# Optimization experiments

Measured on AMD Instinct MI355X. Metric: run time of the kernel, lower is better.

Reference implementation:

```python
import jax, jax.numpy as jnp
import numpy as np

H = 16      # num_heads
D = 64      # nhid (per-head dim)
SL, BS = 1024, 64
DM = 1024   # keys_dim == query_dim == values_dim

def setup_inputs() -> dict:
    key = jax.random.key(0)
    k1, k2, k3, k4, k5 = jax.random.split(key, 5)
    return {
        "query":  jax.random.normal(k1, (BS, DM), dtype=jnp.float32),
        "keys":   jax.random.normal(k2, (SL, BS, DM), dtype=jnp.float32),
        "values": jax.random.normal(k3, (SL, BS, DM), dtype=jnp.float32),
        "Wq":     jax.random.normal(k4, (H * D, DM), dtype=jnp.float32) * 0.02,
        "Wk":     jax.random.normal(k5, (H * D, DM), dtype=jnp.float32) * 0.02,
    }

def reference(query, keys, values, Wq, Wk):
    bs = query.shape[0]
    sl = keys.shape[0]
    scale = jnp.asarray(np.sqrt(D), dtype=query.dtype)
    # projections (note: original module applies keys_linear to values -- a bug we replicate)
    qp = (query @ Wq.T).reshape(bs, H, D)                 # [bs, H, D]
    kp = (keys @ Wk.T).reshape(sl, bs, H, D)              # [sl, bs, H, D]
    vp = (values @ Wk.T).reshape(sl, bs, H, D)            # [sl, bs, H, D]
    # per-head scaled dot-product scores, softmax over the sequence axis (dim 0)
    scores = jnp.einsum('bhd,sbhd->sbh', qp, kp) / scale  # [sl, bs, H]
    attn = jax.nn.softmax(scores, axis=0)
    out = jnp.einsum('sbh,sbhd->bhd', attn, vp)           # [bs, H, D]
    return out.reshape(bs, H * D)
```

## Files before the change

kernel.cpp:

```cpp
#include <hip/hip_runtime.h>
#include <cstddef>
#include <cstdint>

#define NH 16
#define HD 64
#define SLEN 1024
#define NB 64
#define DMODEL 1024

#define DOT4_ACC(acc, k, q) \
  acc = fmaf((k).x, (q).x, fmaf((k).y, (q).y, fmaf((k).z, (q).z, fmaf((k).w, (q).w, (acc)))))

#define FMA4_BCAST(accv, qv, w0_, w1_, w2_, w3_) do { \
  (accv).x = fmaf((qv).x, (w0_).x, fmaf((qv).y, (w1_).x, fmaf((qv).z, (w2_).x, fmaf((qv).w, (w3_).x, (accv).x)))); \
  (accv).y = fmaf((qv).x, (w0_).y, fmaf((qv).y, (w1_).y, fmaf((qv).z, (w2_).y, fmaf((qv).w, (w3_).y, (accv).y)))); \
  (accv).z = fmaf((qv).x, (w0_).z, fmaf((qv).y, (w1_).z, fmaf((qv).z, (w2_).z, fmaf((qv).w, (w3_).z, (accv).z)))); \
  (accv).w = fmaf((qv).x, (w0_).w, fmaf((qv).y, (w1_).w, fmaf((qv).z, (w2_).w, fmaf((qv).w, (w3_).w, (accv).w)))); \
} while (0)

__device__ __forceinline__ float wred_sum(float v) {
#pragma unroll
  for (int off = 32; off; off >>= 1) v += __shfl_xor(v, off, 64);
  return v;
}

__device__ __forceinline__ void gload16(const float* g, float* lds_base) {
  __builtin_amdgcn_global_load_lds(
      (const __attribute__((address_space(1))) void*)g,
      (__attribute__((address_space(3))) void*)lds_base, 16, 0, 0);
}

__global__ __launch_bounds__(256) void k0_qp(const float* __restrict__ query,
                                             const float* __restrict__ Wq,
                                             float* __restrict__ qp) {
  const int tid = threadIdx.x;
  const int w = tid >> 6, l = tid & 63;
  const int j = blockIdx.x * 4 + w;
  const float4* wr = reinterpret_cast<const float4*>(Wq + (size_t)j * DMODEL) + l * 4;
  const float4 w0 = wr[0], w1 = wr[1], w2 = wr[2], w3 = wr[3];
  for (int b = 0; b < NB; ++b) {
    const float4* qr = reinterpret_cast<const float4*>(query + (size_t)b * DMODEL) + l * 4;
    float4 q0 = qr[0], q1 = qr[1], q2 = qr[2], q3 = qr[3];
    float s = 0.f;
    DOT4_ACC(s, w0, q0); DOT4_ACC(s, w1, q1); DOT4_ACC(s, w2, q2); DOT4_ACC(s, w3, q3);
    s = wred_sum(s);
    if (l == 0) qp[(size_t)b * DMODEL + j] = s;
  }
}

__global__ __launch_bounds__(256) void k1_qt(const float* __restrict__ qp,
                                             const float* __restrict__ Wk,
                                             float* __restrict__ qt) {
  __shared__ __align__(16) float qpl[8][HD];
  const int h = blockIdx.x & 15;
  const int b0 = (blockIdx.x >> 4) * 8;
  const int tid = threadIdx.x;
  for (int f = tid; f < 8 * HD; f += 256) {
    int bi = f >> 6, d = f & 63;
    qpl[bi][d] = qp[(size_t)(b0 + bi) * DMODEL + h * HD + d];
  }
  __syncthreads();
  const int m4 = tid * 4;
  float4 acc[8];
#pragma unroll
  for (int i = 0; i < 8; ++i) acc[i] = make_float4(0.f, 0.f, 0.f, 0.f);
  const float* wbase = Wk + (size_t)(h * HD) * DMODEL + m4;
  for (int d = 0; d < HD; d += 4) {
    float4 wk0 = *reinterpret_cast<const float4*>(wbase + (size_t)(d + 0) * DMODEL);
    float4 wk1 = *reinterpret_cast<const float4*>(wbase + (size_t)(d + 1) * DMODEL);
    float4 wk2 = *reinterpret_cast<const float4*>(wbase + (size_t)(d + 2) * DMODEL);
    float4 wk3 = *reinterpret_cast<const float4*>(wbase + (size_t)(d + 3) * DMODEL);
#pragma unroll
    for (int bi = 0; bi < 8; ++bi) {
      float4 q = *reinterpret_cast<const float4*>(&qpl[bi][d]);
      FMA4_BCAST(acc[bi], q, wk0, wk1, wk2, wk3);
    }
  }
#pragma unroll
  for (int bi = 0; bi < 8; ++bi)
    *reinterpret_cast<float4*>(qt + ((size_t)(b0 + bi) * NH + h) * DMODEL + m4) = acc[bi];
}

__global__ __launch_bounds__(128) void k2_scores(const float* __restrict__ keys,
                                                 const float* __restrict__ qt,
                                                 float* __restrict__ scp) {
  __shared__ __align__(16) float ql[NH][512];
  __shared__ __align__(16) float kb[128 * 16];
  const int b  = blockIdx.x & 63;
  const int st = (blockIdx.x >> 6) & 7;
  const int mh = blockIdx.x >> 9;
  const int tid = threadIdx.x, w = tid >> 6, l = tid & 63;
  const int hg = l & 3;
  const int sg = l >> 2;
  for (int f = tid; f < NH * 128; f += 128) {
    int hh = f >> 7, m4 = (f & 127) * 4;
    *reinterpret_cast<float4*>(&ql[hh][m4]) = *reinterpret_cast<const float4*>(
        qt + ((size_t)b * NH + hh) * DMODEL + mh * 512 + m4);
  }
  const int s0 = st * 128;
  const size_t rowstride = (size_t)NB * DMODEL;
  const float* kbase = keys + ((size_t)s0 * NB + b) * DMODEL + mh * 512;
  const int srow  = l >> 2;
  const int sslot = (l & 3) ^ (srow & 3);
  float acc[4][NH];
#pragma unroll
  for (int si = 0; si < 4; ++si)
#pragma unroll
    for (int hh = 0; hh < NH; ++hh) acc[si][hh] = 0.f;
  const int sl0 = w * 64 + sg;

  for (int ch = 0; ch < 32; ++ch) {
#pragma unroll
    for (int i = 0; i < 4; ++i) {
      const int u = w * 4 + i;
      const int row = u * 16 + srow;
      const float* g = kbase + (size_t)row * rowstride + ch * 16 + sslot * 4;
      gload16(g, &kb[u * 256]);
    }
    __syncthreads();
    float4 kv[4];
#pragma unroll
    for (int si = 0; si < 4; ++si) {
      const int s = sl0 + si * 16;
      kv[si] = *reinterpret_cast<const float4*>(&kb[s * 16 + ((hg ^ (s & 3)) << 2)]);
    }
#pragma unroll
    for (int hh = 0; hh < NH; ++hh) {
      float4 q = *reinterpret_cast<const float4*>(&ql[hh][ch * 16 + hg * 4]);
      DOT4_ACC(acc[0][hh], kv[0], q);
      DOT4_ACC(acc[1][hh], kv[1], q);
      DOT4_ACC(acc[2][hh], kv[2], q);
      DOT4_ACC(acc[3][hh], kv[3], q);
    }
    __syncthreads();
  }
#pragma unroll
  for (int si = 0; si < 4; ++si)
#pragma unroll
    for (int hh = 0; hh < NH; ++hh) {
      acc[si][hh] += __shfl_xor(acc[si][hh], 1, 64);
      acc[si][hh] += __shfl_xor(acc[si][hh], 2, 64);
    }
  const float scale = 0.125f;
  float* plane = scp + (size_t)mh * NB * NH * SLEN;
#pragma unroll
  for (int j = 0; j < 4; ++j) {
#pragma unroll
    for (int si = 0; si < 4; ++si) {
      float r = hg == 0 ? acc[si][j] : hg == 1 ? acc[si][4 + j]
              : hg == 2 ? acc[si][8 + j] : acc[si][12 + j];
      plane[((size_t)b * NH + hg * 4 + j) * SLEN + s0 + sl0 + si * 16] = r * scale;
    }
  }
}

__global__ __launch_bounds__(256) void k_sm(float* __restrict__ sc0,
                                            const float* __restrict__ sc1) {
  __shared__ float red[8];
  const int tid = threadIdx.x, w = tid >> 6, l = tid & 63;
  float* p0 = sc0 + (size_t)blockIdx.x * SLEN;
  const float* p1 = sc1 + (size_t)blockIdx.x * SLEN;
  float4 xa = reinterpret_cast<const float4*>(p0)[tid];
  float4 xb = reinterpret_cast<const float4*>(p1)[tid];
  float4 x = make_float4(xa.x + xb.x, xa.y + xb.y, xa.z + xb.z, xa.w + xb.w);
  float mx = fmaxf(fmaxf(x.x, x.y), fmaxf(x.z, x.w));
#pragma unroll
  for (int off = 32; off; off >>= 1) mx = fmaxf(mx, __shfl_xor(mx, off, 64));
  if (l == 0) red[w] = mx;
  __syncthreads();
  mx = fmaxf(fmaxf(red[0], red[1]), fmaxf(red[2], red[3]));
  float4 e;
  e.x = __expf(x.x - mx); e.y = __expf(x.y - mx);
  e.z = __expf(x.z - mx); e.w = __expf(x.w - mx);
  float sum = e.x + e.y + e.z + e.w;
  sum = wred_sum(sum);
  if (l == 0) red[4 + w] = sum;
  __syncthreads();
  sum = red[4] + red[5] + red[6] + red[7];
  const float inv = 1.f / sum;
  e.x *= inv; e.y *= inv; e.z *= inv; e.w *= inv;
  reinterpret_cast<float4*>(p0)[tid] = e;
}

template <int NCH>
__global__ __launch_bounds__(256) void k3_cpart(const float* __restrict__ values,
                                                const float* __restrict__ attn,
                                                float* __restrict__ cp) {
  constexpr int SC = SLEN / NCH;
  __shared__ __align__(16) float vb[4][DMODEL];
  __shared__ __align__(16) float al[NH][SC];
  const int b = blockIdx.x & 63;
  const int ch = blockIdx.x >> 6;
  const int s0 = ch * SC;
  const int tid = threadIdx.x, w = tid >> 6, l = tid & 63;
  for (int f = tid; f < NH * (SC / 4); f += 256) {
    int hh = f / (SC / 4), c4 = (f % (SC / 4)) * 4;
    *reinterpret_cast<float4*>(&al[hh][c4]) = *reinterpret_cast<const float4*>(
        attn + ((size_t)b * NH + hh) * SLEN + s0 + c4);
  }
  const int m4 = tid * 4;
  float4 acc[NH];
#pragma unroll
  for (int i = 0; i < NH; ++i) acc[i] = make_float4(0.f, 0.f, 0.f, 0.f);
  const size_t rowstride = (size_t)NB * DMODEL;
  const float* vbase = values + ((size_t)s0 * NB + b) * DMODEL;

  for (int g = 0; g < SC / 4; ++g) {
    {
      const float* rg = vbase + (size_t)(g * 4 + w) * rowstride;
#pragma unroll
      for (int j = 0; j < 4; ++j)
        gload16(rg + j * 256 + l * 4, &vb[w][j * 256]);
    }
    __syncthreads();
    float4 v0 = *reinterpret_cast<const float4*>(&vb[0][m4]);
    float4 v1 = *reinterpret_cast<const float4*>(&vb[1][m4]);
    float4 v2 = *reinterpret_cast<const float4*>(&vb[2][m4]);
    float4 v3 = *reinterpret_cast<const float4*>(&vb[3][m4]);
#pragma unroll
    for (int hh = 0; hh < NH; ++hh) {
      float4 av = *reinterpret_cast<const float4*>(&al[hh][g * 4]);
      FMA4_BCAST(acc[hh], av, v0, v1, v2, v3);
    }
    __syncthreads();
  }
#pragma unroll
  for (int hh = 0; hh < NH; ++hh)
    *reinterpret_cast<float4*>(cp + (((size_t)ch * NB + b) * NH + hh) * DMODEL + m4) = acc[hh];
}

template <int NCH>
__global__ __launch_bounds__(256) void k4_out(const float* __restrict__ cp,
                                              const float* __restrict__ Wk,
                                              float* __restrict__ out) {
  __shared__ __align__(16) float cl[4 * DMODEL];
  const int h = blockIdx.x & 15;
  const int b0 = (blockIdx.x >> 4) * 4;
  const int tid = threadIdx.x, w = tid >> 6, l = tid & 63;
  for (int f = tid; f < 4 * DMODEL / 4; f += 256) {
    int bi = f >> 8, m4 = (f & 255) * 4;
    float4 s = make_float4(0.f, 0.f, 0.f, 0.f);
#pragma unroll
    for (int ch = 0; ch < NCH; ++ch) {
      float4 t = *reinterpret_cast<const float4*>(
          cp + (((size_t)ch * NB + b0 + bi) * NH + h) * DMODEL + m4);
      s.x += t.x; s.y += t.y; s.z += t.z; s.w += t.w;
    }
    *reinterpret_cast<float4*>(&cl[bi * DMODEL + m4]) = s;
  }
  __syncthreads();
  float4 c[4][4];
#pragma unroll
  for (int bi = 0; bi < 4; ++bi)
#pragma unroll
    for (int k = 0; k < 4; ++k)
      c[bi][k] = *reinterpret_cast<const float4*>(&cl[bi * DMODEL + l * 16 + k * 4]);
  for (int jj = 0; jj < 16; ++jj) {
    const int d = w * 16 + jj;
    const float4* wr = reinterpret_cast<const float4*>(Wk + (size_t)(h * HD + d) * DMODEL) + l * 4;
    const float4 w0 = wr[0], w1 = wr[1], w2 = wr[2], w3 = wr[3];
#pragma unroll
    for (int bi = 0; bi < 4; ++bi) {
      float s = 0.f;
      DOT4_ACC(s, w0, c[bi][0]); DOT4_ACC(s, w1, c[bi][1]);
      DOT4_ACC(s, w2, c[bi][2]); DOT4_ACC(s, w3, c[bi][3]);
      s = wred_sum(s);
      if (l == 0) out[(size_t)(b0 + bi) * (NH * HD) + h * HD + d] = s;
    }
  }
}

extern "C" void kernel_launch(void* const* d_in, const int* in_sizes, int n_in,
                              void* d_out, int out_size, void* d_ws, size_t ws_size,
                              hipStream_t stream) {
  const float* query  = (const float*)d_in[0];
  const float* keys   = (const float*)d_in[1];
  const float* values = (const float*)d_in[2];
  const float* Wq     = (const float*)d_in[3];
  const float* Wk     = (const float*)d_in[4];
  float* out = (float*)d_out;

  float* W   = (float*)d_ws;
  float* qp  = W;
  float* qt  = qp + (size_t)NB * DMODEL;
  float* sc0 = qt + (size_t)NB * NH * DMODEL;
  float* sc1 = sc0 + (size_t)NB * NH * SLEN;
  float* cp  = sc1 + (size_t)NB * NH * SLEN;

  const size_t base_floats = (size_t)NB * DMODEL + (size_t)NB * NH * DMODEL
                           + 2 * (size_t)NB * NH * SLEN;

  k0_qp<<<256, 256, 0, stream>>>(query, Wq, qp);
  k1_qt<<<128, 256, 0, stream>>>(qp, Wk, qt);
  k2_scores<<<1024, 128, 0, stream>>>(keys, qt, sc0);
  k_sm<<<NB * NH, 256, 0, stream>>>(sc0, sc1);

  const size_t chunk_floats = (size_t)NB * NH * DMODEL;
  if (ws_size >= (base_floats + 16 * chunk_floats) * sizeof(float)) {
    k3_cpart<16><<<16 * NB, 256, 0, stream>>>(values, sc0, cp);
    k4_out<16><<<NH * (NB / 4), 256, 0, stream>>>(cp, Wk, out);
  } else if (ws_size >= (base_floats + 8 * chunk_floats) * sizeof(float)) {
    k3_cpart<8><<<8 * NB, 256, 0, stream>>>(values, sc0, cp);
    k4_out<8><<<NH * (NB / 4), 256, 0, stream>>>(cp, Wk, out);
  } else {
    k3_cpart<4><<<4 * NB, 256, 0, stream>>>(values, sc0, cp);
    k4_out<4><<<NH * (NB / 4), 256, 0, stream>>>(cp, Wk, out);
  }
}
```

Baseline: 255.4 us.

## Double-buffer key/value LDS staging in scores and context kernels

Both the scores kernel and the context-partial kernel now use two LDS buffers. The next chunk's global-to-LDS loads are issued before computing on the current chunk, so memory latency overlaps with the FMA work. The scores kernel also stops preloading the full 16x512 query slice and instead streams a small per-chunk query tile alongside the keys, which cuts its LDS footprint and may raise occupancy. In exchange, k3 uses twice the LDS for its value buffer, which could lower its occupancy. Correctness also depends on the barrier waiting for the outstanding async loads.

```diff
diff --git a/kernel.cpp b/kernel.cpp
--- a/kernel.cpp
+++ b/kernel.cpp
@@ -84,24 +84,35 @@
 __global__ __launch_bounds__(128) void k2_scores(const float* __restrict__ keys,
                                                  const float* __restrict__ qt,
                                                  float* __restrict__ scp) {
-  __shared__ __align__(16) float ql[NH][512];
-  __shared__ __align__(16) float kb[128 * 16];
+  __shared__ __align__(16) float kb[2][128 * 16];
+  __shared__ __align__(16) float qb[2][NH * 16];
   const int b  = blockIdx.x & 63;
   const int st = (blockIdx.x >> 6) & 7;
   const int mh = blockIdx.x >> 9;
   const int tid = threadIdx.x, w = tid >> 6, l = tid & 63;
   const int hg = l & 3;
   const int sg = l >> 2;
-  for (int f = tid; f < NH * 128; f += 128) {
-    int hh = f >> 7, m4 = (f & 127) * 4;
-    *reinterpret_cast<float4*>(&ql[hh][m4]) = *reinterpret_cast<const float4*>(
-        qt + ((size_t)b * NH + hh) * DMODEL + mh * 512 + m4);
-  }
   const int s0 = st * 128;
   const size_t rowstride = (size_t)NB * DMODEL;
   const float* kbase = keys + ((size_t)s0 * NB + b) * DMODEL + mh * 512;
+  const float* qbase = qt + (size_t)b * NH * DMODEL + mh * 512;
   const int srow  = l >> 2;
   const int sslot = (l & 3) ^ (srow & 3);
+  const int qh = l >> 2, qj = l & 3;
+
+#define K2_STAGE(buf_, ch_) do {                                              \
+    _Pragma("unroll")                                                         \
+    for (int i_ = 0; i_ < 4; ++i_) {                                          \
+      const int u_ = w * 4 + i_;                                              \
+      const int row_ = u_ * 16 + srow;                                        \
+      gload16(kbase + (size_t)row_ * rowstride + (ch_) * 16 + sslot * 4,      \
+              &kb[buf_][u_ * 256]);                                           \
+    }                                                                         \
+    if (w == 0)                                                               \
+      gload16(qbase + (size_t)qh * DMODEL + (ch_) * 16 + qj * 4,              \
+              &qb[buf_][0]);                                                  \
+  } while (0)
+
   float acc[4][NH];
 #pragma unroll
   for (int si = 0; si < 4; ++si)
@@ -109,24 +120,20 @@
     for (int hh = 0; hh < NH; ++hh) acc[si][hh] = 0.f;
   const int sl0 = w * 64 + sg;
 
+  K2_STAGE(0, 0);
+  __syncthreads();
   for (int ch = 0; ch < 32; ++ch) {
-#pragma unroll
-    for (int i = 0; i < 4; ++i) {
-      const int u = w * 4 + i;
-      const int row = u * 16 + srow;
-      const float* g = kbase + (size_t)row * rowstride + ch * 16 + sslot * 4;
-      gload16(g, &kb[u * 256]);
-    }
-    __syncthreads();
+    const int buf = ch & 1;
+    if (ch + 1 < 32) K2_STAGE(buf ^ 1, ch + 1);
     float4 kv[4];
 #pragma unroll
     for (int si = 0; si < 4; ++si) {
       const int s = sl0 + si * 16;
-      kv[si] = *reinterpret_cast<const float4*>(&kb[s * 16 + ((hg ^ (s & 3)) << 2)]);
+      kv[si] = *reinterpret_cast<const float4*>(&kb[buf][s * 16 + ((hg ^ (s & 3)) << 2)]);
     }
 #pragma unroll
     for (int hh = 0; hh < NH; ++hh) {
-      float4 q = *reinterpret_cast<const float4*>(&ql[hh][ch * 16 + hg * 4]);
+      float4 q = *reinterpret_cast<const float4*>(&qb[buf][hh * 16 + hg * 4]);
       DOT4_ACC(acc[0][hh], kv[0], q);
       DOT4_ACC(acc[1][hh], kv[1], q);
       DOT4_ACC(acc[2][hh], kv[2], q);
@@ -134,6 +141,7 @@
     }
     __syncthreads();
   }
+#undef K2_STAGE
 #pragma unroll
   for (int si = 0; si < 4; ++si)
 #pragma unroll
@@ -187,7 +195,7 @@
                                                 const float* __restrict__ attn,
                                                 float* __restrict__ cp) {
   constexpr int SC = SLEN / NCH;
-  __shared__ __align__(16) float vb[4][DMODEL];
+  __shared__ __align__(16) float vb[2][4][DMODEL];
   __shared__ __align__(16) float al[NH][SC];
   const int b = blockIdx.x & 63;
   const int ch = blockIdx.x >> 6;
@@ -205,18 +213,22 @@
   const size_t rowstride = (size_t)NB * DMODEL;
   const float* vbase = values + ((size_t)s0 * NB + b) * DMODEL;
 
+#define K3_STAGE(buf_, g_) do {                                               \
+    const float* rg_ = vbase + (size_t)((g_) * 4 + w) * rowstride;            \
+    _Pragma("unroll")                                                         \
+    for (int j_ = 0; j_ < 4; ++j_)                                            \
+      gload16(rg_ + j_ * 256 + l * 4, &vb[buf_][w][j_ * 256]);                \
+  } while (0)
+
+  K3_STAGE(0, 0);
+  __syncthreads();
   for (int g = 0; g < SC / 4; ++g) {
-    {
-      const float* rg = vbase + (size_t)(g * 4 + w) * rowstride;
-#pragma unroll
-      for (int j = 0; j < 4; ++j)
-        gload16(rg + j * 256 + l * 4, &vb[w][j * 256]);
-    }
-    __syncthreads();
-    float4 v0 = *reinterpret_cast<const float4*>(&vb[0][m4]);
-    float4 v1 = *reinterpret_cast<const float4*>(&vb[1][m4]);
-    float4 v2 = *reinterpret_cast<const float4*>(&vb[2][m4]);
-    float4 v3 = *reinterpret_cast<const float4*>(&vb[3][m4]);
+    const int buf = g & 1;
+    if (g + 1 < SC / 4) K3_STAGE(buf ^ 1, g + 1);
+    float4 v0 = *reinterpret_cast<const float4*>(&vb[buf][0][m4]);
+    float4 v1 = *reinterpret_cast<const float4*>(&vb[buf][1][m4]);
+    float4 v2 = *reinterpret_cast<const float4*>(&vb[buf][2][m4]);
+    float4 v3 = *reinterpret_cast<const float4*>(&vb[buf][3][m4]);
 #pragma unroll
     for (int hh = 0; hh < NH; ++hh) {
       float4 av = *reinterpret_cast<const float4*>(&al[hh][g * 4]);
@@ -224,6 +236,7 @@
     }
     __syncthreads();
   }
+#undef K3_STAGE
 #pragma unroll
   for (int hh = 0; hh < NH; ++hh)
     *reinterpret_cast<float4*>(cp + (((size_t)ch * NB + b) * NH + hh) * DMODEL + m4) = acc[hh];
```

Result: faster. 250.2 us (-2.1%).
